# Performance work log

Measured on AMD Instinct MI355X. Metric: run time of the kernel, lower is better.

Reference implementation:

```python
import jax, jax.numpy as jnp
import numpy as np

B, S, DIM, H, HD, K, DEPTH = 2, 2048, 1024, 16, 64, 64, 8
SCALE = 1.0 / np.sqrt(HD)


def _build_cantor_routes(seq_len: int, k: int, depth: int) -> np.ndarray:
    # Vectorized version of CantorAttention._build_cantor_routes
    pos = np.arange(seq_len, dtype=np.float64)
    x = pos / max(1, seq_len - 1)
    x = np.clip(x, 1e-06, 1.0 - 1e-06)
    cantor = np.zeros(seq_len, dtype=np.float64)
    factor = 0.5
    for _ in range(depth):
        x = x * 3.0
        digit = np.floor(x)
        x = x - digit
        cantor += factor * (digit == 2.0)
        factor *= 0.5
    cantor = cantor.astype(np.float32)
    # k nearest positions in Cantor space for each position
    dist = np.abs(cantor[:, None] - cantor[None, :])  # [S, S]
    routes = np.argsort(dist, axis=1, kind='stable')[:, :k]  # [S, k]
    return routes.astype(np.int32)


def setup_inputs() -> dict:
    key = jax.random.key(0)
    k1, k2, k3, k4, k5 = jax.random.split(key, 5)
    s = 1.0 / np.sqrt(DIM)
    return {
        'x': jax.random.normal(k1, (B, S, DIM), dtype=jnp.float32),
        'w_qkv': jax.random.normal(k2, (3 * DIM, DIM), dtype=jnp.float32) * s,
        'b_qkv': jax.random.normal(k3, (3 * DIM,), dtype=jnp.float32) * 0.01,
        'w_out': jax.random.normal(k4, (DIM, DIM), dtype=jnp.float32) * s,
        'b_out': jax.random.normal(k5, (DIM,), dtype=jnp.float32) * 0.01,
        'routes': jnp.asarray(_build_cantor_routes(S, K, DEPTH)),
    }


def reference(x, w_qkv, b_qkv, w_out, b_out, routes):
    b, s, _ = x.shape
    # QKV projection (torch Linear: y = x @ W.T + b)
    qkv = x @ w_qkv.T + b_qkv                       # [B, S, 3*DIM]
    qkv = qkv.reshape(b, s, 3, H, HD).transpose(2, 0, 3, 1, 4)  # [3, B, H, S, HD]
    q, k, v = qkv[0], qkv[1], qkv[2]                # each [B, H, S, HD]
    # Gather k/v at Cantor neighbor routes: [B, H, S, K, HD]
    k_g = jnp.take(k, routes, axis=2)
    v_g = jnp.take(v, routes, axis=2)
    scores = jnp.einsum('bhqd,bhqkd->bhqk', q, k_g) * SCALE
    attn = jax.nn.softmax(scores, axis=-1)
    out = jnp.einsum('bhqk,bhqkd->bhqd', attn, v_g)  # [B, H, S, HD]
    out = out.transpose(0, 2, 1, 3).reshape(b, s, DIM)
    return out @ w_out.T + b_out
```

## Files before the change

### kernel.cpp

```cpp
#include <hip/hip_runtime.h>

#define BQ   2
#define SQ   2048
#define DIMQ 1024
#define HQ   16
#define HDQ  64
#define KQ   64
#define QKV_STRIDE (3 * DIMQ)

typedef __attribute__((ext_vector_type(8))) short short8;
typedef __attribute__((ext_vector_type(4))) float floatx4;

typedef const __attribute__((address_space(1))) unsigned short* gas_t;
typedef __attribute__((address_space(3))) unsigned short* las_t;

__device__ __forceinline__ unsigned short f2b(float f) {
    union { float f; unsigned int u; } x; x.f = f;
    unsigned int r = x.u + 0x7fffu + ((x.u >> 16) & 1u);
    return (unsigned short)(r >> 16);
}
__device__ __forceinline__ float b2f(unsigned short u) {
    union { unsigned int u; float f; } x; x.u = ((unsigned int)u) << 16;
    return x.f;
}

__global__ __launch_bounds__(256) void cast3_f32_bf16(const float* __restrict__ s0, unsigned short* __restrict__ d0, int n0,
                                                      const float* __restrict__ s1, unsigned short* __restrict__ d1, int n1,
                                                      const float* __restrict__ s2, unsigned short* __restrict__ d2, int n2) {
    int i = blockIdx.x * blockDim.x + threadIdx.x;
    const float* s; unsigned short* d;
    if (i < n0)                { s = s0; d = d0; }
    else if (i < n0 + n1)      { s = s1; d = d1; i -= n0; }
    else if (i < n0 + n1 + n2) { s = s2; d = d2; i -= n0 + n1; }
    else return;
    float4 v = ((const float4*)s)[i];
    ushort4 o;
    o.x = f2b(v.x); o.y = f2b(v.y); o.z = f2b(v.z); o.w = f2b(v.w);
    ((ushort4*)d)[i] = o;
}

template <int BM, int BN, typename CT>
__global__ __launch_bounds__(256) void gemm_bf16_nt(const unsigned short* __restrict__ A,
                                                    const unsigned short* __restrict__ B,
                                                    const float* __restrict__ bias,
                                                    CT* __restrict__ C,
                                                    int M, int N, int K) {
    constexpr int MI = BM / 32;
    constexpr int NJ = BN / 32;
    __shared__ unsigned short As[BM * 32];
    __shared__ unsigned short Bs[BN * 32];

    const int tid  = threadIdx.x;
    const int lane = tid & 63;
    const int wv   = tid >> 6;
    const int wm   = (wv >> 1) * (BM / 2);
    const int wn   = (wv & 1) * (BN / 2);
    const int fr   = lane & 15;
    const int fq   = lane >> 4;

    const int m0 = blockIdx.y * BM;
    const int n0 = blockIdx.x * BN;

    floatx4 acc[MI][NJ];
#pragma unroll
    for (int i = 0; i < MI; ++i)
#pragma unroll
        for (int j = 0; j < NJ; ++j) acc[i][j] = (floatx4)(0.f);

    const unsigned short* Ab = A + (size_t)m0 * K;
    const unsigned short* Bb = B + (size_t)n0 * K;

    for (int k0 = 0; k0 < K; k0 += 32) {
#pragma unroll
        for (int c = 0; c < (BM + BN) * 4; c += 256) {
            const int cc = c + tid;
            if (cc < BM * 4) {
                __builtin_amdgcn_global_load_lds(
                    (gas_t)(Ab + (size_t)(cc >> 2) * K + k0 + ((cc & 3) << 3)),
                    (las_t)&As[cc * 8], 16, 0, 0);
            } else {
                const int c2 = cc - BM * 4;
                __builtin_amdgcn_global_load_lds(
                    (gas_t)(Bb + (size_t)(c2 >> 2) * K + k0 + ((c2 & 3) << 3)),
                    (las_t)&Bs[c2 * 8], 16, 0, 0);
            }
        }
        __syncthreads();

        short8 af[MI], bf[NJ];
#pragma unroll
        for (int i = 0; i < MI; ++i)
            af[i] = *(const short8*)&As[(wm + i * 16 + fr) * 32 + fq * 8];
#pragma unroll
        for (int j = 0; j < NJ; ++j)
            bf[j] = *(const short8*)&Bs[(wn + j * 16 + fr) * 32 + fq * 8];
#pragma unroll
        for (int i = 0; i < MI; ++i)
#pragma unroll
            for (int j = 0; j < NJ; ++j)
                acc[i][j] = __builtin_amdgcn_mfma_f32_16x16x32_bf16(af[i], bf[j], acc[i][j], 0, 0, 0);
        __syncthreads();
    }

    float bv[NJ];
#pragma unroll
    for (int j = 0; j < NJ; ++j) bv[j] = bias[n0 + wn + j * 16 + fr];
#pragma unroll
    for (int i = 0; i < MI; ++i) {
#pragma unroll
        for (int r = 0; r < 4; ++r) {
            const size_t row = (size_t)(m0 + wm + i * 16 + fq * 4 + r);
#pragma unroll
            for (int j = 0; j < NJ; ++j) {
                const float v = acc[i][j][r] + bv[j];
                if constexpr (sizeof(CT) == 2)
                    C[row * N + n0 + wn + j * 16 + fr] = (CT)f2b(v);
                else
                    C[row * N + n0 + wn + j * 16 + fr] = (CT)v;
            }
        }
    }
}

__global__ __launch_bounds__(256) void attn_kernel(const unsigned short* __restrict__ qkv,
                                                   const int* __restrict__ routes,
                                                   unsigned short* __restrict__ out) {
    __shared__ int   r_s[KQ];
    __shared__ float m_s[128], l_s[128];
    __shared__ float o_part[8][128];

    const int t  = threadIdx.x;
    const int id = blockIdx.x;
    const int bq = (id & 7) * 512 + (id >> 3);
    const int b  = bq >> 11;
    const int q  = bq & 2047;

    if (t < KQ) r_s[t] = routes[q * KQ + t];

    const int g  = t >> 7;
    const int th = t & 127;
    const int h  = th >> 3;
    const int d0 = (t & 7) * 8;

    float qf[8];
    {
        const short8 q8 = *(const short8*)&qkv[((size_t)bq * 3) * DIMQ + h * HDQ + d0];
#pragma unroll
        for (int e = 0; e < 8; ++e) qf[e] = b2f((unsigned short)q8[e]);
    }
    __syncthreads();

    const size_t baseK = ((size_t)b * SQ * 3 + 1) * DIMQ + h * HDQ + d0;
    const size_t baseV = ((size_t)b * SQ * 3 + 2) * DIMQ + h * HDQ + d0;

    float m = -1e30f, l = 0.f;
    float o[8];
#pragma unroll
    for (int e = 0; e < 8; ++e) o[e] = 0.f;

#pragma unroll 4
    for (int jj = 0; jj < KQ / 2; ++jj) {
        const int j = jj * 2 + g;
        const size_t roff = (size_t)r_s[j] * QKV_STRIDE;
        const short8 k8 = *(const short8*)&qkv[baseK + roff];
        const short8 v8 = *(const short8*)&qkv[baseV + roff];
        float p = 0.f;
#pragma unroll
        for (int e = 0; e < 8; ++e) p += qf[e] * b2f((unsigned short)k8[e]);
        p += __shfl_xor(p, 1, 64);
        p += __shfl_xor(p, 2, 64);
        p += __shfl_xor(p, 4, 64);
        const float s  = p * 0.125f;
        const float mn = fmaxf(m, s);
        const float al = __expf(m - mn);
        const float pe = __expf(s - mn);
        l = l * al + pe;
#pragma unroll
        for (int e = 0; e < 8; ++e) o[e] = o[e] * al + pe * b2f((unsigned short)v8[e]);
        m = mn;
    }

    if (g == 1) {
        m_s[th] = m; l_s[th] = l;
#pragma unroll
        for (int e = 0; e < 8; ++e) o_part[e][th] = o[e];
    }
    __syncthreads();
    if (g == 0) {
        const float m1 = m_s[th], l1 = l_s[th];
        const float mm = fmaxf(m, m1);
        const float a0 = __expf(m - mm);
        const float a1 = __expf(m1 - mm);
        const float inv = 1.0f / (l * a0 + l1 * a1);
        float oo[8];
#pragma unroll
        for (int e = 0; e < 8; ++e) oo[e] = (o[e] * a0 + o_part[e][th] * a1) * inv;
        ushort4 lo, hi;
        lo.x = f2b(oo[0]); lo.y = f2b(oo[1]); lo.z = f2b(oo[2]); lo.w = f2b(oo[3]);
        hi.x = f2b(oo[4]); hi.y = f2b(oo[5]); hi.z = f2b(oo[6]); hi.w = f2b(oo[7]);
        ushort4* dst = (ushort4*)&out[(size_t)bq * DIMQ + h * HDQ + d0];
        dst[0] = lo; dst[1] = hi;
    }
}

extern "C" void kernel_launch(void* const* d_in, const int* in_sizes, int n_in,
                              void* d_out, int out_size, void* d_ws, size_t ws_size,
                              hipStream_t stream) {
    const float* x      = (const float*)d_in[0];
    const float* w_qkv  = (const float*)d_in[1];
    const float* b_qkv  = (const float*)d_in[2];
    const float* w_out  = (const float*)d_in[3];
    const float* b_out  = (const float*)d_in[4];
    const int*   routes = (const int*)d_in[5];
    float* out = (float*)d_out;

    char* ws = (char*)d_ws;
    unsigned short* qkvb  = (unsigned short*)ws;
    unsigned short* xb    = (unsigned short*)(ws + 25165824);
    unsigned short* attnb = xb;
    unsigned short* wqb   = (unsigned short*)(ws + 33554432);
    unsigned short* wob   = (unsigned short*)(ws + 39845888);

    const int M = BQ * SQ;
    dim3 blk(256);

    {
        const int n0 = M * DIMQ / 4, n1 = 3 * DIMQ * DIMQ / 4, n2 = DIMQ * DIMQ / 4;
        cast3_f32_bf16<<<(n0 + n1 + n2 + 255) / 256, blk, 0, stream>>>(
            x, xb, n0, w_qkv, wqb, n1, w_out, wob, n2);
    }

    gemm_bf16_nt<128, 128, unsigned short><<<dim3(3 * DIMQ / 128, M / 128), blk, 0, stream>>>(
        xb, wqb, b_qkv, qkvb, M, 3 * DIMQ, DIMQ);

    attn_kernel<<<BQ * SQ, blk, 0, stream>>>(qkvb, routes, attnb);

    gemm_bf16_nt<128, 64, float><<<dim3(DIMQ / 64, M / 128), blk, 0, stream>>>(
        attnb, wob, b_out, out, M, DIMQ, DIMQ);
}
```

Measured before the change: 202.3 us.

## Compute attention scores with masked MFMA and use an explicit softmax

New measurement: 223.5 us. 1.1x slower.

```diff
diff --git a/kernel.cpp b/kernel.cpp
--- a/kernel.cpp
+++ b/kernel.cpp
@@ -125,80 +125,109 @@
 __global__ __launch_bounds__(256) void attn_kernel(const unsigned short* __restrict__ qkv,
                                                    const int* __restrict__ routes,
                                                    unsigned short* __restrict__ out) {
+    __shared__ unsigned short q_lds[DIMQ];
     __shared__ int   r_s[KQ];
-    __shared__ float m_s[128], l_s[128];
+    __shared__ float s_s[HQ][KQ + 1];
     __shared__ float o_part[8][128];
 
-    const int t  = threadIdx.x;
-    const int id = blockIdx.x;
+    const int t    = threadIdx.x;
+    const int lane = t & 63;
+    const int wv   = t >> 6;
+    const int id   = blockIdx.x;
     const int bq = (id & 7) * 512 + (id >> 3);
     const int b  = bq >> 11;
     const int q  = bq & 2047;
 
+    if (wv < 2) {
+        __builtin_amdgcn_global_load_lds(
+            (gas_t)(qkv + (size_t)bq * 3 * DIMQ + wv * 512 + lane * 8),
+            (las_t)&q_lds[wv * 512], 16, 0, 0);
+    }
     if (t < KQ) r_s[t] = routes[q * KQ + t];
+    __syncthreads();
+
+    {
+        const int fm = lane & 15;
+        const int kh = lane >> 4;
+        const int rA = r_s[wv * 16 + fm];
+        const unsigned short* Abase =
+            qkv + ((size_t)b * SQ * 3 + 1) * DIMQ + (size_t)rA * QKV_STRIDE + kh * 8;
+        const unsigned short* qbase = &q_lds[kh * 8];
+
+        floatx4 accS = (floatx4)(0.f);
+        const short8 z8 = (short8)0;
+#pragma unroll
+        for (int hh = 0; hh < HQ; ++hh) {
+            const short8 a0 = *(const short8*)(Abase + hh * 64);
+            const short8 a1 = *(const short8*)(Abase + hh * 64 + 32);
+            short8 b0 = *(const short8*)(qbase + hh * 64);
+            short8 b1 = *(const short8*)(qbase + hh * 64 + 32);
+            if (fm != hh) { b0 = z8; b1 = z8; }
+            accS = __builtin_amdgcn_mfma_f32_16x16x32_bf16(a0, b0, accS, 0, 0, 0);
+            accS = __builtin_amdgcn_mfma_f32_16x16x32_bf16(a1, b1, accS, 0, 0, 0);
+        }
+#pragma unroll
+        for (int r = 0; r < 4; ++r)
+            s_s[fm][wv * 16 + kh * 4 + r] = accS[r] * 0.125f;
+    }
+    __syncthreads();
+
+    {
+        const int sh = ((t >> 6) << 2) + ((t & 63) >> 4);
+        const int i  = t & 15;
+        float v0 = s_s[sh][i], v1 = s_s[sh][i + 16], v2 = s_s[sh][i + 32], v3 = s_s[sh][i + 48];
+        float mx = fmaxf(fmaxf(v0, v1), fmaxf(v2, v3));
+        mx = fmaxf(mx, __shfl_xor(mx, 1, 64));
+        mx = fmaxf(mx, __shfl_xor(mx, 2, 64));
+        mx = fmaxf(mx, __shfl_xor(mx, 4, 64));
+        mx = fmaxf(mx, __shfl_xor(mx, 8, 64));
+        float e0 = __expf(v0 - mx), e1 = __expf(v1 - mx);
+        float e2 = __expf(v2 - mx), e3 = __expf(v3 - mx);
+        float sm = e0 + e1 + e2 + e3;
+        sm += __shfl_xor(sm, 1, 64);
+        sm += __shfl_xor(sm, 2, 64);
+        sm += __shfl_xor(sm, 4, 64);
+        sm += __shfl_xor(sm, 8, 64);
+        const float inv = 1.0f / sm;
+        s_s[sh][i]      = e0 * inv;
+        s_s[sh][i + 16] = e1 * inv;
+        s_s[sh][i + 32] = e2 * inv;
+        s_s[sh][i + 48] = e3 * inv;
+    }
+    __syncthreads();
 
     const int g  = t >> 7;
     const int th = t & 127;
-    const int h  = th >> 3;
+    const int h2 = th >> 3;
     const int d0 = (t & 7) * 8;
 
-    float qf[8];
-    {
-        const short8 q8 = *(const short8*)&qkv[((size_t)bq * 3) * DIMQ + h * HDQ + d0];
-#pragma unroll
-        for (int e = 0; e < 8; ++e) qf[e] = b2f((unsigned short)q8[e]);
-    }
-    __syncthreads();
-
-    const size_t baseK = ((size_t)b * SQ * 3 + 1) * DIMQ + h * HDQ + d0;
-    const size_t baseV = ((size_t)b * SQ * 3 + 2) * DIMQ + h * HDQ + d0;
-
-    float m = -1e30f, l = 0.f;
+    const size_t baseV = ((size_t)b * SQ * 3 + 2) * DIMQ + h2 * HDQ + d0;
     float o[8];
 #pragma unroll
     for (int e = 0; e < 8; ++e) o[e] = 0.f;
 
 #pragma unroll 4
     for (int jj = 0; jj < KQ / 2; ++jj) {
-        const int j = jj * 2 + g;
-        const size_t roff = (size_t)r_s[j] * QKV_STRIDE;
-        const short8 k8 = *(const short8*)&qkv[baseK + roff];
-        const short8 v8 = *(const short8*)&qkv[baseV + roff];
-        float p = 0.f;
-#pragma unroll
-        for (int e = 0; e < 8; ++e) p += qf[e] * b2f((unsigned short)k8[e]);
-        p += __shfl_xor(p, 1, 64);
-        p += __shfl_xor(p, 2, 64);
-        p += __shfl_xor(p, 4, 64);
-        const float s  = p * 0.125f;
-        const float mn = fmaxf(m, s);
-        const float al = __expf(m - mn);
-        const float pe = __expf(s - mn);
-        l = l * al + pe;
-#pragma unroll
-        for (int e = 0; e < 8; ++e) o[e] = o[e] * al + pe * b2f((unsigned short)v8[e]);
-        m = mn;
+        const int   j = jj * 2 + g;
+        const int   r = r_s[j];
+        const float w = s_s[h2][j];
+        const short8 v8 = *(const short8*)&qkv[baseV + (size_t)r * QKV_STRIDE];
+#pragma unroll
+        for (int e = 0; e < 8; ++e) o[e] += w * b2f((unsigned short)v8[e]);
     }
 
     if (g == 1) {
-        m_s[th] = m; l_s[th] = l;
 #pragma unroll
         for (int e = 0; e < 8; ++e) o_part[e][th] = o[e];
     }
     __syncthreads();
     if (g == 0) {
-        const float m1 = m_s[th], l1 = l_s[th];
-        const float mm = fmaxf(m, m1);
-        const float a0 = __expf(m - mm);
-        const float a1 = __expf(m1 - mm);
-        const float inv = 1.0f / (l * a0 + l1 * a1);
-        float oo[8];
-#pragma unroll
-        for (int e = 0; e < 8; ++e) oo[e] = (o[e] * a0 + o_part[e][th] * a1) * inv;
         ushort4 lo, hi;
-        lo.x = f2b(oo[0]); lo.y = f2b(oo[1]); lo.z = f2b(oo[2]); lo.w = f2b(oo[3]);
-        hi.x = f2b(oo[4]); hi.y = f2b(oo[5]); hi.z = f2b(oo[6]); hi.w = f2b(oo[7]);
-        ushort4* dst = (ushort4*)&out[(size_t)bq * DIMQ + h * HDQ + d0];
+        lo.x = f2b(o[0] + o_part[0][th]); lo.y = f2b(o[1] + o_part[1][th]);
+        lo.z = f2b(o[2] + o_part[2][th]); lo.w = f2b(o[3] + o_part[3][th]);
+        hi.x = f2b(o[4] + o_part[4][th]); hi.y = f2b(o[5] + o_part[5][th]);
+        hi.z = f2b(o[6] + o_part[6][th]); hi.w = f2b(o[7] + o_part[7][th]);
+        ushort4* dst = (ushort4*)&out[(size_t)bq * DIMQ + h2 * HDQ + d0];
         dst[0] = lo; dst[1] = hi;
     }
 }
```
